# Kernel optimization log

Measured on AMD Instinct MI355X. Metric: run time of the kernel, lower is better.

## Reference

```python
import jax, jax.numpy as jnp
import numpy as np

# edge types from metadata: (src_type, 'to', dst_type)
NODE_SRC = [0, 1, 2, 3, 0, 1, 2, 1, 3, 1]
NODE_DST = [0, 1, 2, 3, 1, 0, 1, 2, 1, 3]
N_NODES = 30000
N_EDGES = 400000
HEADS1 = 8


def _han_conv(xs, edges, proj_W, proj_b, att_src, att_dst, k_W, k_b, q, heads):
    """Faithful port of torch_geometric HANConv (eval mode, dropout off)."""
    out_ch = proj_W.shape[-1]
    D = out_ch // heads
    N = xs[0].shape[0]
    # per-node-type projection -> [N, H, D]
    h = [(xs[t] @ proj_W[t] + proj_b[t]).reshape(N, heads, D) for t in range(4)]
    outs = {t: [] for t in range(4)}
    for e in range(10):
        s, d = NODE_SRC[e], NODE_DST[e]
        row, col = edges[e, 0], edges[e, 1]
        a_src = (h[s] * att_src[e]).sum(-1)  # [N, H]
        a_dst = (h[d] * att_dst[e]).sum(-1)  # [N, H]
        alpha = jax.nn.leaky_relu(a_src[row] + a_dst[col], 0.2)  # [E, H]
        # segment softmax over incoming edges of each dst node
        amax = jax.ops.segment_max(alpha, col, num_segments=N)
        ex = jnp.exp(alpha - amax[col])
        denom = jax.ops.segment_sum(ex, col, num_segments=N)
        w = ex / (denom[col] + 1e-16)
        msg = h[s][row] * w[:, :, None]  # [E, H, D]
        agg = jax.ops.segment_sum(msg, col, num_segments=N).reshape(N, out_ch)
        outs[d].append(jax.nn.relu(agg))
    # semantic-level attention fusion across relations ending at each node type
    res = []
    for t in range(4):
        stk = jnp.stack(outs[t])  # [M, N, C]
        score = (q * jnp.tanh(stk @ k_W + k_b).mean(axis=1)).sum(-1)  # [M]
        sattn = jax.nn.softmax(score)
        res.append((sattn[:, None, None] * stk).sum(0))  # [N, C]
    return res


def setup_inputs() -> dict:
    key = jax.random.key(0)
    ks = jax.random.split(key, 24)
    inp = {}
    for t in range(4):
        inp[f"x{t}"] = jax.random.normal(ks[t], (N_NODES, 256), dtype=jnp.float32)
    inp["edges"] = jax.random.randint(ks[4], (10, 2, N_EDGES), 0, N_NODES, dtype=jnp.int32)
    s = 0.05
    inp["proj1_W"] = jax.random.normal(ks[5], (4, 256, 128), dtype=jnp.float32) * s
    inp["proj1_b"] = jax.random.normal(ks[6], (4, 128), dtype=jnp.float32) * s
    inp["att1_src"] = jax.random.normal(ks[7], (10, 8, 16), dtype=jnp.float32) * s
    inp["att1_dst"] = jax.random.normal(ks[8], (10, 8, 16), dtype=jnp.float32) * s
    inp["k1_W"] = jax.random.normal(ks[9], (128, 128), dtype=jnp.float32) * s
    inp["k1_b"] = jax.random.normal(ks[10], (128,), dtype=jnp.float32) * s
    inp["q1"] = jax.random.normal(ks[11], (128,), dtype=jnp.float32) * s
    inp["proj2_W"] = jax.random.normal(ks[12], (4, 128, 32), dtype=jnp.float32) * s
    inp["proj2_b"] = jax.random.normal(ks[13], (4, 32), dtype=jnp.float32) * s
    inp["att2_src"] = jax.random.normal(ks[14], (10, 1, 32), dtype=jnp.float32) * s
    inp["att2_dst"] = jax.random.normal(ks[15], (10, 1, 32), dtype=jnp.float32) * s
    inp["k2_W"] = jax.random.normal(ks[16], (32, 32), dtype=jnp.float32) * s
    inp["k2_b"] = jax.random.normal(ks[17], (32,), dtype=jnp.float32) * s
    inp["q2"] = jax.random.normal(ks[18], (32,), dtype=jnp.float32) * s
    return inp


def reference(x0, x1, x2, x3, edges,
              proj1_W, proj1_b, att1_src, att1_dst, k1_W, k1_b, q1,
              proj2_W, proj2_b, att2_src, att2_dst, k2_W, k2_b, q2):
    # eval mode: all F.dropout calls are identity
    xs = [x0, x1, x2, x3]
    h = _han_conv(xs, edges, proj1_W, proj1_b, att1_src, att1_dst, k1_W, k1_b, q1, HEADS1)
    h = [jax.nn.elu(v) for v in h]
    o = _han_conv(h, edges, proj2_W, proj2_b, att2_src, att2_dst, k2_W, k2_b, q2, 1)
    # final per-node softmax over channel dim for each node type; stack since all N equal
    return jnp.stack([jax.nn.softmax(v, axis=1) for v in o])  # [4, N, 32]
```

## Files before the change

### kernel.cpp

```cpp
#include <hip/hip_runtime.h>
#include <hip/hip_fp16.h>

#define NN 30000
#define NE 400000
#define NBUCK 59
#define BPR 98
#define EPB 4096
#define CAPREG 12288
#define BCAP 12288

__constant__ int d_SRC[10] = {0,1,2,3,0,1,2,1,3,1};
__constant__ int d_DST[10] = {0,1,2,3,1,0,1,2,1,3};
__constant__ int d_RORD[10] = {1,5,7,9,0,4,2,6,3,8};
__constant__ int d_GORD[10] = {0,4,1,5,7,9,2,6,3,8};
__constant__ int d_FCNT[4] = {2,4,2,2};
__constant__ int d_FREL[4][4] = {{0,5,0,0},{1,4,6,8},{2,7,0,0},{3,9,0,0}};

typedef _Float16 f16x8 __attribute__((ext_vector_type(8)));
typedef float f32x4 __attribute__((ext_vector_type(4)));

template<int BN, bool AF16>
__global__ __launch_bounds__(256)
void mgemm_k(const float* __restrict__ A, long sA,
             const float* __restrict__ B, long sB,
             const float* __restrict__ bias, long sBias,
             float* __restrict__ C, long sC,
             int M, int K, int N, int relu_a, int epi)
{
    constexpr int BM = 64, BK = 32;
    constexpr int NF = BN / 16;
    constexpr int LDK = BK + 8;
    const int z = blockIdx.z;
    const _Float16* __restrict__ Ah = (const _Float16*)A;
    if constexpr (AF16) Ah += (long)z * sA; else A += (long)z * sA;
    B += (long)z * sB;
    bias += (long)z * sBias;
    C += (long)z * sC;
    const int m0 = blockIdx.x * BM;
    const int n0 = blockIdx.y * BN;
    const int tid = threadIdx.x;
    const int wv = tid >> 6;
    const int l  = tid & 63;
    const int fm = l & 15;
    const int fg = l >> 4;

    __shared__ _Float16 As[BM][LDK];
    __shared__ _Float16 Bs[BN][LDK];
    __shared__ float red[4][BN];

    f32x4 acc[NF];
#pragma unroll
    for (int f = 0; f < NF; ++f) acc[f] = (f32x4){0.f, 0.f, 0.f, 0.f};

    const int arow = tid >> 2;
    const int akc  = (tid & 3) << 3;
    const int grow = m0 + arow;

    for (int k0 = 0; k0 < K; k0 += BK) {
        f16x8 ap;
        if (grow < M) {
            if constexpr (AF16) {
                ap = *(const f16x8*)(Ah + (long)grow * K + k0 + akc);
                if (relu_a) {
#pragma unroll
                    for (int j = 0; j < 8; ++j)
                        ap[j] = ap[j] > (_Float16)0.f ? ap[j] : (_Float16)0.f;
                }
            } else {
                const float* aq = A + (long)grow * K + k0 + akc;
                float4 u0 = *(const float4*)aq;
                float4 u1 = *(const float4*)(aq + 4);
                float v[8] = {u0.x, u0.y, u0.z, u0.w, u1.x, u1.y, u1.z, u1.w};
                if (relu_a) {
#pragma unroll
                    for (int j = 0; j < 8; ++j) v[j] = fmaxf(v[j], 0.f);
                }
#pragma unroll
                for (int j = 0; j < 8; ++j) ap[j] = (_Float16)v[j];
            }
        } else {
#pragma unroll
            for (int j = 0; j < 8; ++j) ap[j] = (_Float16)0.f;
        }
        *(f16x8*)&As[arow][akc] = ap;

        if constexpr (BN == 64) {
            const int bk = tid >> 4;
            const int bn = (tid & 15) << 2;
#pragma unroll
            for (int kk = 0; kk < 2; ++kk) {
                int kr = bk + kk * 16;
                float4 u = *(const float4*)(B + (long)(k0 + kr) * N + n0 + bn);
                Bs[bn + 0][kr] = (_Float16)u.x;
                Bs[bn + 1][kr] = (_Float16)u.y;
                Bs[bn + 2][kr] = (_Float16)u.z;
                Bs[bn + 3][kr] = (_Float16)u.w;
            }
        } else {
            const int bk = tid >> 3;
            const int bn = (tid & 7) << 2;
            float4 u = *(const float4*)(B + (long)(k0 + bk) * N + n0 + bn);
            Bs[bn + 0][bk] = (_Float16)u.x;
            Bs[bn + 1][bk] = (_Float16)u.y;
            Bs[bn + 2][bk] = (_Float16)u.z;
            Bs[bn + 3][bk] = (_Float16)u.w;
        }
        __syncthreads();

        f16x8 a = *(const f16x8*)&As[wv * 16 + fm][fg * 8];
#pragma unroll
        for (int f = 0; f < NF; ++f) {
            f16x8 b = *(const f16x8*)&Bs[f * 16 + fm][fg * 8];
            acc[f] = __builtin_amdgcn_mfma_f32_16x16x32_f16(a, b, acc[f], 0, 0, 0);
        }
        __syncthreads();
    }

    if (epi == 0) {
#pragma unroll
        for (int f = 0; f < NF; ++f) {
            float bz = bias[n0 + f * 16 + fm];
#pragma unroll
            for (int i = 0; i < 4; ++i) {
                int gr = m0 + wv * 16 + fg * 4 + i;
                if (gr < M) C[(long)gr * N + n0 + f * 16 + fm] = acc[f][i] + bz;
            }
        }
    } else if (epi == 2) {
        __half* Ch = (__half*)C;
#pragma unroll
        for (int f = 0; f < NF; ++f) {
            float bz = bias[n0 + f * 16 + fm];
#pragma unroll
            for (int i = 0; i < 4; ++i) {
                int gr = m0 + wv * 16 + fg * 4 + i;
                if (gr < M) Ch[(long)gr * N + n0 + f * 16 + fm] = __float2half(acc[f][i] + bz);
            }
        }
    } else {
#pragma unroll
        for (int f = 0; f < NF; ++f) {
            float bz = bias[n0 + f * 16 + fm];
            float s = 0.f;
#pragma unroll
            for (int i = 0; i < 4; ++i) {
                int gr = m0 + wv * 16 + fg * 4 + i;
                if (gr < M) s += tanhf(acc[f][i] + bz);
            }
            s += __shfl_xor(s, 16, 64);
            s += __shfl_xor(s, 32, 64);
            if (fg == 0) red[wv][f * 16 + fm] = s;
        }
        __syncthreads();
        if (tid < BN) {
            float s = red[0][tid] + red[1][tid] + red[2][tid] + red[3][tid];
            unsafeAtomicAdd(&C[n0 + tid], s);
        }
    }
}

__global__ __launch_bounds__(256)
void init_bincur(int* __restrict__ binCur)
{
    int i = blockIdx.x * 256 + threadIdx.x;
    if (i < 10 * NBUCK) binCur[i] = (i % NBUCK) * CAPREG;
}

__global__ __launch_bounds__(256)
void csr_binA(const int* __restrict__ edges, int* __restrict__ binCur,
              unsigned* __restrict__ binned)
{
    __shared__ int lcnt[NBUCK];
    __shared__ int gbase[NBUCK];
    int rel = blockIdx.x / BPR;
    int blk = blockIdx.x - rel * BPR;
    int base = blk * EPB;
    int tid = threadIdx.x;
    for (int b = tid; b < NBUCK; b += 256) lcnt[b] = 0;
    __syncthreads();
    const int* er = edges + (long)rel * 2 * NE;
    const int* ec = er + NE;
    unsigned pk[16];
    unsigned mt[16];
#pragma unroll
    for (int k = 0; k < 16; ++k) {
        int i = base + k * 256 + tid;
        if (i < NE) {
            int r = er[i];
            int c = ec[i];
            int b = c >> 9;
            int lo = atomicAdd(&lcnt[b], 1);
            pk[k] = ((unsigned)c << 15) | (unsigned)r;
            mt[k] = ((unsigned)b << 16) | (unsigned)lo;
        } else {
            mt[k] = 0xFFFFFFFFu;
        }
    }
    __syncthreads();
    if (tid < NBUCK) gbase[tid] = atomicAdd(&binCur[rel * NBUCK + tid], lcnt[tid]);
    __syncthreads();
    unsigned* bn = binned + (long)rel * NBUCK * CAPREG;
#pragma unroll
    for (int k = 0; k < 16; ++k) {
        if (mt[k] != 0xFFFFFFFFu) {
            int b = mt[k] >> 16;
            int lo = mt[k] & 0xFFFF;
            bn[gbase[b] + lo] = pk[k];
        }
    }
}

__global__ __launch_bounds__(64)
void bucket_scan(const int* __restrict__ binCur, int* __restrict__ bbase,
                 int* __restrict__ off_all)
{
    int rel = blockIdx.x;
    int t = threadIdx.x;
    __shared__ int c[64];
    int v = (t < NBUCK) ? (binCur[rel * NBUCK + t] - t * CAPREG) : 0;
    c[t] = v;
    __syncthreads();
    for (int d = 1; d < 64; d <<= 1) {
        int u = (t >= d) ? c[t - d] : 0;
        __syncthreads();
        c[t] += u;
        __syncthreads();
    }
    if (t < NBUCK) bbase[rel * NBUCK + t] = c[t] - v;
    if (t == 0) off_all[rel * (NN + 1) + NN] = NE;
}

__global__ __launch_bounds__(256)
void csr_binB(const int* __restrict__ binCur, const int* __restrict__ bbase,
              const unsigned* __restrict__ binned,
              int* __restrict__ off_all, int* __restrict__ rows)
{
    __shared__ int cntS[512];
    __shared__ int lcur[512];
    __shared__ int part[256];
    __shared__ int buf[BCAP];
    int rel = blockIdx.x / NBUCK;
    int bkt = blockIdx.x - rel * NBUCK;
    const unsigned* bn = binned + ((long)rel * NBUCK + bkt) * CAPREG;
    int* off = off_all + rel * (NN + 1);
    int* rw = rows + (long)rel * NE;
    int cnt = binCur[rel * NBUCK + bkt] - bkt * CAPREG;
    int gbase = bbase[rel * NBUCK + bkt];
    int nb0 = bkt << 9;
    int nb1 = min(nb0 + 512, NN);
    int nloc = nb1 - nb0;
    int tid = threadIdx.x;

    cntS[tid] = 0; cntS[tid + 256] = 0;
    __syncthreads();
    for (int j = tid; j < cnt; j += 256) {
        int c = (int)(bn[j] >> 15);
        atomicAdd(&cntS[c - nb0], 1);
    }
    __syncthreads();
    int c0 = cntS[2 * tid], c1 = cntS[2 * tid + 1];
    part[tid] = c0 + c1;
    __syncthreads();
    for (int d = 1; d < 256; d <<= 1) {
        int u = (tid >= d) ? part[tid - d] : 0;
        __syncthreads();
        part[tid] += u;
        __syncthreads();
    }
    int pre = (tid == 0) ? 0 : part[tid - 1];
    cntS[2 * tid] = pre;
    cntS[2 * tid + 1] = pre + c0;
    __syncthreads();
    for (int i = tid; i < nloc; i += 256) off[nb0 + i] = gbase + cntS[i];
    lcur[tid] = cntS[tid]; lcur[tid + 256] = cntS[tid + 256];
    __syncthreads();
    if (cnt <= BCAP) {
        for (int j = tid; j < cnt; j += 256) {
            unsigned p = bn[j];
            int r = (int)(p & 0x7FFF);
            int c = (int)(p >> 15);
            int pos = atomicAdd(&lcur[c - nb0], 1);
            buf[pos] = r;
        }
        __syncthreads();
        for (int i = tid; i < cnt; i += 256) rw[gbase + i] = buf[i];
    } else {
        for (int j = tid; j < cnt; j += 256) {
            unsigned p = bn[j];
            int r = (int)(p & 0x7FFF);
            int c = (int)(p >> 15);
            int pos = atomicAdd(&lcur[c - nb0], 1);
            rw[gbase + pos] = r;
        }
    }
}

__global__ __launch_bounds__(256)
void attn_dots1(const __half* __restrict__ h1h,
                const float* __restrict__ att_src,
                const float* __restrict__ att_dst,
                float* __restrict__ asrc, float* __restrict__ adst)
{
    int gid = blockIdx.x * 256 + threadIdx.x;
    int wave = gid >> 6;
    int lane = gid & 63;
    if (wave >= 4 * NN) return;
    int t = wave / NN;
    int n = wave - t * NN;
    __half2 hh = *(const __half2*)&h1h[(long)(t * NN + n) * 128 + 2 * lane];
    float2 hv = __half22float2(hh);
    const int SRCc[10] = {0,1,2,3,0,1,2,1,3,1};
    const int DSTc[10] = {0,1,2,3,1,0,1,2,1,3};
#pragma unroll
    for (int e = 0; e < 10; ++e) {
        if (SRCc[e] == t) {
            float2 av = *(const float2*)&att_src[e * 128 + 2 * lane];
            float p = hv.x * av.x + hv.y * av.y;
#pragma unroll
            for (int off = 1; off < 8; off <<= 1) p += __shfl_xor(p, off, 64);
            if ((lane & 7) == 0) asrc[(long)(e * NN + n) * 8 + (lane >> 3)] = p;
        }
        if (DSTc[e] == t) {
            float2 bv = *(const float2*)&att_dst[e * 128 + 2 * lane];
            float p = hv.x * bv.x + hv.y * bv.y;
#pragma unroll
            for (int off = 1; off < 8; off <<= 1) p += __shfl_xor(p, off, 64);
            if ((lane & 7) == 0) adst[(long)(e * NN + n) * 8 + (lane >> 3)] = p;
        }
    }
}

__global__ __launch_bounds__(256)
void gather_agg1_all(const int* __restrict__ csr_off, const int* __restrict__ csr_rows,
                     const float* __restrict__ asrc1, const float* __restrict__ adst1,
                     const __half* __restrict__ h1h, __half* __restrict__ slots16)
{
    int e = d_GORD[blockIdx.y];
    int node = blockIdx.x * 4 + (threadIdx.x >> 6);
    int lane = threadIdx.x & 63;
    if (node >= NN) return;
    const int* off = csr_off + e * (NN + 1);
    const int* rows = csr_rows + (long)e * NE;
    const float* asrc_e = asrc1 + (long)e * NN * 8;
    const float* adst_e = adst1 + (long)e * NN * 8;
    const __half* h1s = h1h + (long)d_SRC[e] * NN * 128;
    __half* out = slots16 + (long)e * NN * 128;

    const int hB = lane >> 3;
    const int hA = lane & 7;
    const int eA = lane >> 3;
    int beg = off[node], end = off[node + 1];
    float adA = adst_e[node * 8 + hA];
    float den = 1e-16f;
    float accx = 0.f, accy = 0.f;
    for (int j0 = beg; j0 < end; j0 += 8) {
        int jj = j0 + eA;
        bool ok = jj < end;
        int r = rows[ok ? jj : beg];
        float a = asrc_e[r * 8 + hA] + adA;
        a = a > 0.f ? a : 0.2f * a;
        float w = ok ? __expf(a) : 0.f;
        int cnt = end - j0;
        if (cnt >= 8) {
#pragma unroll
            for (int i = 0; i < 8; ++i) {
                float wi = __shfl(w, i * 8 + hB, 64);
                int ri = __shfl(r, i * 8, 64);
                float2 v = __half22float2(*(const __half2*)&h1s[(long)ri * 128 + 2 * lane]);
                den += wi;
                accx += wi * v.x;
                accy += wi * v.y;
            }
        } else {
            for (int i = 0; i < cnt; ++i) {
                float wi = __shfl(w, i * 8 + hB, 64);
                int ri = __shfl(r, i * 8, 64);
                float2 v = __half22float2(*(const __half2*)&h1s[(long)ri * 128 + 2 * lane]);
                den += wi;
                accx += wi * v.x;
                accy += wi * v.y;
            }
        }
    }
    float inv = 1.0f / den;
    *(__half2*)&out[(long)node * 128 + 2 * lane] = __floats2half2_rn(accx * inv, accy * inv);
}

__global__ __launch_bounds__(256)
void fusion_all(const __half* __restrict__ slots16, const float* __restrict__ sattn,
                __half* __restrict__ h1f)
{
    int t = blockIdx.y;
    int idx = blockIdx.x * 256 + threadIdx.x;
    if (idx >= NN * 32) return;
    int c4 = idx & 31;
    int n = idx >> 5;
    long off = (long)n * 128 + c4 * 4;
    int cnt = d_FCNT[t];
    float o0 = 0.f, o1 = 0.f, o2 = 0.f, o3 = 0.f;
    for (int j = 0; j < cnt; ++j) {
        int e = d_FREL[t][j];
        float w = sattn[e];
        const __half* p = slots16 + (long)e * NN * 128 + off;
        float2 v01 = __half22float2(*(const __half2*)p);
        float2 v23 = __half22float2(*(const __half2*)(p + 2));
        o0 += w * fmaxf(v01.x, 0.f);
        o1 += w * fmaxf(v01.y, 0.f);
        o2 += w * fmaxf(v23.x, 0.f);
        o3 += w * fmaxf(v23.y, 0.f);
    }
    o0 = o0 > 0.f ? o0 : __expf(o0) - 1.f;
    o1 = o1 > 0.f ? o1 : __expf(o1) - 1.f;
    o2 = o2 > 0.f ? o2 : __expf(o2) - 1.f;
    o3 = o3 > 0.f ? o3 : __expf(o3) - 1.f;
    __half* q = h1f + (long)t * NN * 128 + off;
    *(__half2*)q = __floats2half2_rn(o0, o1);
    *(__half2*)(q + 2) = __floats2half2_rn(o2, o3);
}

__global__ __launch_bounds__(256)
void attn_dots2(const __half* __restrict__ h2h,
                const float* __restrict__ att_src,
                const float* __restrict__ att_dst,
                float* __restrict__ asrc, float* __restrict__ adst)
{
    int gid = blockIdx.x * 256 + threadIdx.x;
    int p = gid >> 5;
    int l = gid & 31;
    if (p >= 10 * NN) return;
    int e = p / NN, n = p - e * NN;
    int s = d_SRC[e], d = d_DST[e];
    float hs = __half2float(h2h[(long)(s * NN + n) * 32 + l]);
    float hd = __half2float(h2h[(long)(d * NN + n) * 32 + l]);
    float ps = hs * att_src[e * 32 + l];
    float pd = hd * att_dst[e * 32 + l];
#pragma unroll
    for (int off = 1; off < 32; off <<= 1) {
        ps += __shfl_xor(ps, off, 64);
        pd += __shfl_xor(pd, off, 64);
    }
    if (l == 0) { asrc[e * NN + n] = ps; adst[e * NN + n] = pd; }
}

__global__ __launch_bounds__(256)
void gather_agg2(const int* __restrict__ csr_off, const int* __restrict__ csr_rows,
                 const __half* __restrict__ h2h,
                 const float* __restrict__ asrc, const float* __restrict__ adst,
                 float* __restrict__ agg2)
{
    int e = d_RORD[blockIdx.y];
    int node = blockIdx.x * 8 + (threadIdx.x >> 5);
    int lane = threadIdx.x & 31;
    if (node >= NN) return;
    const int* off = csr_off + e * (NN + 1);
    const int* rows = csr_rows + (long)e * NE;
    const __half* h2s = h2h + (long)d_SRC[e] * NN * 32;
    const float* as = asrc + e * NN;
    float ad = adst[e * NN + node];
    int beg = off[node], end = off[node + 1];
    float den = 1e-16f;
    float acc = 0.f;
    for (int j0 = beg; j0 < end; j0 += 32) {
        int jj = j0 + lane;
        bool ok = jj < end;
        int r = rows[ok ? jj : beg];
        float a = as[r] + ad;
        a = a > 0.f ? a : 0.2f * a;
        float w = ok ? __expf(a) : 0.f;
        int cnt = min(32, end - j0);
        int i = 0;
        for (; i + 3 < cnt; i += 4) {
            float w0 = __shfl(w, i, 32);
            float w1 = __shfl(w, i + 1, 32);
            float w2 = __shfl(w, i + 2, 32);
            float w3 = __shfl(w, i + 3, 32);
            int r0 = __shfl(r, i, 32);
            int r1 = __shfl(r, i + 1, 32);
            int r2 = __shfl(r, i + 2, 32);
            int r3 = __shfl(r, i + 3, 32);
            float v0 = __half2float(h2s[(long)r0 * 32 + lane]);
            float v1 = __half2float(h2s[(long)r1 * 32 + lane]);
            float v2 = __half2float(h2s[(long)r2 * 32 + lane]);
            float v3 = __half2float(h2s[(long)r3 * 32 + lane]);
            den += (w0 + w1) + (w2 + w3);
            acc += w0 * v0 + w1 * v1 + w2 * v2 + w3 * v3;
        }
        for (; i < cnt; ++i) {
            float wi = __shfl(w, i, 32);
            int ri = __shfl(r, i, 32);
            den += wi;
            acc += wi * __half2float(h2s[(long)ri * 32 + lane]);
        }
    }
    agg2[((long)e * NN + node) * 32 + lane] = acc / den;
}

__global__ void score_all_k(const float* __restrict__ colsum, const float* __restrict__ q,
                            float* __restrict__ sattn, int C)
{
    __shared__ float sc[10];
    int tid = threadIdx.x;
    if (tid < 10) {
        float s = 0.f;
        for (int c = 0; c < C; ++c) s += q[c] * colsum[tid * C + c];
        sc[tid] = s / (float)NN;
    }
    __syncthreads();
    if (tid < 4) {
        float mx = -1e30f;
        for (int m = 0; m < 10; ++m) if (d_DST[m] == tid) mx = fmaxf(mx, sc[m]);
        float ex[10];
        float sum = 0.f;
        for (int m = 0; m < 10; ++m) {
            ex[m] = 0.f;
            if (d_DST[m] == tid) { ex[m] = __expf(sc[m] - mx); sum += ex[m]; }
        }
        for (int m = 0; m < 10; ++m) if (d_DST[m] == tid) sattn[m] = ex[m] / sum;
    }
}

__global__ __launch_bounds__(256)
void final_softmax(const float* __restrict__ agg, const float* __restrict__ sattn,
                   float* __restrict__ out)
{
    int gid = blockIdx.x * 256 + threadIdx.x;
    int c = gid & 31;
    int p = gid >> 5;
    if (p >= 4 * NN) return;
    int t = p / NN, n = p - t * NN;
    float f = 0.f;
    for (int m = 0; m < 10; ++m) {
        if (d_DST[m] != t) continue;
        f += sattn[m] * fmaxf(agg[(long)(m * NN + n) * 32 + c], 0.f);
    }
    float mx = f;
#pragma unroll
    for (int off = 1; off < 32; off <<= 1) mx = fmaxf(mx, __shfl_xor(mx, off, 64));
    float ex = __expf(f - mx);
    float sm = ex;
#pragma unroll
    for (int off = 1; off < 32; off <<= 1) sm += __shfl_xor(sm, off, 64);
    out[(long)(t * NN + n) * 32 + c] = ex / sm;
}

extern "C" void kernel_launch(void* const* d_in, const int* in_sizes, int n_in,
                              void* d_out, int out_size, void* d_ws, size_t ws_size,
                              hipStream_t stream) {
    const float* x[4] = {
        (const float*)d_in[0], (const float*)d_in[1],
        (const float*)d_in[2], (const float*)d_in[3]};
    const int* edges = (const int*)d_in[4];
    const float* W1    = (const float*)d_in[5];
    const float* b1    = (const float*)d_in[6];
    const float* att1s = (const float*)d_in[7];
    const float* att1d = (const float*)d_in[8];
    const float* k1W   = (const float*)d_in[9];
    const float* k1b   = (const float*)d_in[10];
    const float* q1    = (const float*)d_in[11];
    const float* W2    = (const float*)d_in[12];
    const float* b2    = (const float*)d_in[13];
    const float* att2s = (const float*)d_in[14];
    const float* att2d = (const float*)d_in[15];
    const float* k2W   = (const float*)d_in[16];
    const float* k2b   = (const float*)d_in[17];
    const float* q2    = (const float*)d_in[18];

    float* W = (float*)d_ws;
    __half* h1h    = (__half*)W;
    __half* h1f    = (__half*)W;
    __half* h2h    = (__half*)(W + 7680000);
    __half* slots16 = (__half*)(W + 15360000);
    float* agg2    = W + 15360000;
    unsigned* binned = (unsigned*)(W + 15360000);
    int*   binCur  = (int*)(W + 15360000 + 7249920);
    int*   bbase   = binCur + 640;
    float* asrc1   = W + 34560000;
    float* adst1   = W + 36960000;
    float* asrc2   = W + 36960000;
    float* adst2   = W + 37260000;
    float* colsum1 = W + 39360000;
    float* sattn1  = W + 39361280;
    float* colsum2 = W + 39361296;
    float* sattn2  = W + 39361616;
    int*   csr_off = (int*)(W + 39361640);
    int*   csr_row = csr_off + 300016;

    init_bincur<<<3, 256, 0, stream>>>(binCur);
    csr_binA<<<BPR * 10, 256, 0, stream>>>(edges, binCur, binned);
    bucket_scan<<<10, 64, 0, stream>>>(binCur, bbase, csr_off);
    csr_binB<<<NBUCK * 10, 256, 0, stream>>>(binCur, bbase, binned, csr_off, csr_row);

    hipMemsetAsync(colsum1, 0, 1632L * 4, stream);

    for (int t = 0; t < 4; ++t) {
        mgemm_k<64, false><<<dim3(469, 2, 1), 256, 0, stream>>>(
            x[t], 0, W1 + (long)t * 256 * 128, 0, b1 + t * 128, 0,
            (float*)(h1h + (long)t * NN * 128), 0, NN, 256, 128, 0, 2);
    }

    attn_dots1<<<30000, 256, 0, stream>>>(h1h, att1s, att1d, asrc1, adst1);

    gather_agg1_all<<<dim3(7500, 10), 256, 0, stream>>>(
        csr_off, csr_row, asrc1, adst1, h1h, slots16);

    mgemm_k<64, true><<<dim3(469, 2, 10), 256, 0, stream>>>(
        (const float*)slots16, (long)NN * 128, k1W, 0, k1b, 0,
        colsum1, 128, NN, 128, 128, 1, 1);
    score_all_k<<<1, 64, 0, stream>>>(colsum1, q1, sattn1, 128);

    fusion_all<<<dim3(3750, 4), 256, 0, stream>>>(slots16, sattn1, h1f);

    mgemm_k<32, true><<<dim3(469, 1, 4), 256, 0, stream>>>(
        (const float*)h1f, (long)NN * 128, W2, 128L * 32, b2, 32,
        (float*)h2h, (long)NN * 16, NN, 128, 32, 0, 2);

    attn_dots2<<<37500, 256, 0, stream>>>(h2h, att2s, att2d, asrc2, adst2);
    gather_agg2<<<dim3(3750, 10), 256, 0, stream>>>(
        csr_off, csr_row, h2h, asrc2, adst2, agg2);

    mgemm_k<32, false><<<dim3(469, 1, 10), 256, 0, stream>>>(
        agg2, 960000L, k2W, 0, k2b, 0, colsum2, 32L, NN, 32, 32, 1, 1);
    score_all_k<<<1, 64, 0, stream>>>(colsum2, q2, sattn2, 32);
    final_softmax<<<15000, 256, 0, stream>>>(agg2, sattn2, (float*)d_out);
}
```

Measured before the change: 801.8 us.

## Widen gather loads to 8 bytes and store layer-2 aggregates in fp16

In layer 1, the gather kernel now splits each 64-lane wave into two half-waves that take alternate edges, each lane loading four fp16 values, and combines the halves with a cross-lane shuffle. The layer-2 gather moves from one 32-lane group per node to one 64-lane wave per node, with eight edge slots of eight lanes each, 8-byte loads and a shuffle reduction. The layer-2 aggregate buffer changes from fp32 to fp16, so the following GEMM and the final softmax read half the bytes. The aim is fewer, wider memory transactions and less traffic, at the cost of extra shuffle reductions, idle lanes on low-degree nodes, and fp16 rounding of the layer-2 aggregates.

```diff
diff --git a/kernel.cpp b/kernel.cpp
--- a/kernel.cpp
+++ b/kernel.cpp
@@ -18,6 +18,8 @@
 
 typedef _Float16 f16x8 __attribute__((ext_vector_type(8)));
 typedef float f32x4 __attribute__((ext_vector_type(4)));
+
+struct __attribute__((aligned(8))) h2x2 { __half2 a, b; };
 
 template<int BN, bool AF16>
 __global__ __launch_bounds__(256)
@@ -346,13 +348,28 @@
     const __half* h1s = h1h + (long)d_SRC[e] * NN * 128;
     __half* out = slots16 + (long)e * NN * 128;
 
-    const int hB = lane >> 3;
-    const int hA = lane & 7;
-    const int eA = lane >> 3;
+    const int g   = lane >> 5;
+    const int sub = lane & 31;
+    const int hv  = sub >> 2;
+    const int eA  = lane >> 3;
+    const int hA  = lane & 7;
     int beg = off[node], end = off[node + 1];
     float adA = adst_e[node * 8 + hA];
-    float den = 1e-16f;
-    float accx = 0.f, accy = 0.f;
+    float den = (g == 0) ? 1e-16f : 0.f;
+    float a0 = 0.f, a1 = 0.f, a2 = 0.f, a3 = 0.f;
+
+#define GA1_PAIR(i)                                                              \
+    {                                                                            \
+        int e0 = 2 * (i) + g;                                                    \
+        float wi = __shfl(w, e0 * 8 + hv, 64);                                   \
+        int ri = __shfl(r, e0 * 8, 64);                                          \
+        h2x2 v = *(const h2x2*)(h1s + (long)ri * 128 + 4 * sub);                 \
+        float2 f0 = __half22float2(v.a);                                         \
+        float2 f1 = __half22float2(v.b);                                         \
+        den += wi;                                                               \
+        a0 += wi * f0.x; a1 += wi * f0.y; a2 += wi * f1.x; a3 += wi * f1.y;      \
+    }
+
     for (int j0 = beg; j0 < end; j0 += 8) {
         int jj = j0 + eA;
         bool ok = jj < end;
@@ -362,28 +379,25 @@
         float w = ok ? __expf(a) : 0.f;
         int cnt = end - j0;
         if (cnt >= 8) {
-#pragma unroll
-            for (int i = 0; i < 8; ++i) {
-                float wi = __shfl(w, i * 8 + hB, 64);
-                int ri = __shfl(r, i * 8, 64);
-                float2 v = __half22float2(*(const __half2*)&h1s[(long)ri * 128 + 2 * lane]);
-                den += wi;
-                accx += wi * v.x;
-                accy += wi * v.y;
-            }
+            GA1_PAIR(0) GA1_PAIR(1) GA1_PAIR(2) GA1_PAIR(3)
         } else {
-            for (int i = 0; i < cnt; ++i) {
-                float wi = __shfl(w, i * 8 + hB, 64);
-                int ri = __shfl(r, i * 8, 64);
-                float2 v = __half22float2(*(const __half2*)&h1s[(long)ri * 128 + 2 * lane]);
-                den += wi;
-                accx += wi * v.x;
-                accy += wi * v.y;
-            }
-        }
-    }
-    float inv = 1.0f / den;
-    *(__half2*)&out[(long)node * 128 + 2 * lane] = __floats2half2_rn(accx * inv, accy * inv);
+            int pr = (cnt + 1) >> 1;
+            for (int i = 0; i < pr; ++i) GA1_PAIR(i)
+        }
+    }
+#undef GA1_PAIR
+    a0 += __shfl_xor(a0, 32, 64);
+    a1 += __shfl_xor(a1, 32, 64);
+    a2 += __shfl_xor(a2, 32, 64);
+    a3 += __shfl_xor(a3, 32, 64);
+    den += __shfl_xor(den, 32, 64);
+    if (g == 0) {
+        float inv = 1.0f / den;
+        h2x2 o;
+        o.a = __floats2half2_rn(a0 * inv, a1 * inv);
+        o.b = __floats2half2_rn(a2 * inv, a3 * inv);
+        *(h2x2*)(out + (long)node * 128 + 4 * sub) = o;
+    }
 }
 
 __global__ __launch_bounds__(256)
@@ -446,53 +460,67 @@
 void gather_agg2(const int* __restrict__ csr_off, const int* __restrict__ csr_rows,
                  const __half* __restrict__ h2h,
                  const float* __restrict__ asrc, const float* __restrict__ adst,
-                 float* __restrict__ agg2)
+                 __half* __restrict__ agg2h)
 {
     int e = d_RORD[blockIdx.y];
-    int node = blockIdx.x * 8 + (threadIdx.x >> 5);
-    int lane = threadIdx.x & 31;
+    int node = blockIdx.x * 4 + (threadIdx.x >> 6);
+    int lane = threadIdx.x & 63;
     if (node >= NN) return;
     const int* off = csr_off + e * (NN + 1);
     const int* rows = csr_rows + (long)e * NE;
     const __half* h2s = h2h + (long)d_SRC[e] * NN * 32;
     const float* as = asrc + e * NN;
+    const int slot = lane >> 3;
+    const int sub = lane & 7;
     float ad = adst[e * NN + node];
     int beg = off[node], end = off[node + 1];
-    float den = 1e-16f;
-    float acc = 0.f;
-    for (int j0 = beg; j0 < end; j0 += 32) {
+    float den = (lane < 8) ? 1e-16f : 0.f;
+    float a0 = 0.f, a1 = 0.f, a2 = 0.f, a3 = 0.f;
+
+#define GA2_STEP(i)                                                              \
+    {                                                                            \
+        int e0 = (i) * 8 + slot;                                                 \
+        float wi = __shfl(w, e0, 64);                                            \
+        int ri = __shfl(r, e0, 64);                                              \
+        h2x2 v = *(const h2x2*)(h2s + (long)ri * 32 + 4 * sub);                  \
+        float2 f0 = __half22float2(v.a);                                         \
+        float2 f1 = __half22float2(v.b);                                         \
+        den += wi;                                                               \
+        a0 += wi * f0.x; a1 += wi * f0.y; a2 += wi * f1.x; a3 += wi * f1.y;      \
+    }
+
+    for (int j0 = beg; j0 < end; j0 += 64) {
         int jj = j0 + lane;
         bool ok = jj < end;
         int r = rows[ok ? jj : beg];
         float a = as[r] + ad;
         a = a > 0.f ? a : 0.2f * a;
         float w = ok ? __expf(a) : 0.f;
-        int cnt = min(32, end - j0);
-        int i = 0;
-        for (; i + 3 < cnt; i += 4) {
-            float w0 = __shfl(w, i, 32);
-            float w1 = __shfl(w, i + 1, 32);
-            float w2 = __shfl(w, i + 2, 32);
-            float w3 = __shfl(w, i + 3, 32);
-            int r0 = __shfl(r, i, 32);
-            int r1 = __shfl(r, i + 1, 32);
-            int r2 = __shfl(r, i + 2, 32);
-            int r3 = __shfl(r, i + 3, 32);
-            float v0 = __half2float(h2s[(long)r0 * 32 + lane]);
-            float v1 = __half2float(h2s[(long)r1 * 32 + lane]);
-            float v2 = __half2float(h2s[(long)r2 * 32 + lane]);
-            float v3 = __half2float(h2s[(long)r3 * 32 + lane]);
-            den += (w0 + w1) + (w2 + w3);
-            acc += w0 * v0 + w1 * v1 + w2 * v2 + w3 * v3;
-        }
-        for (; i < cnt; ++i) {
-            float wi = __shfl(w, i, 32);
-            int ri = __shfl(r, i, 32);
-            den += wi;
-            acc += wi * __half2float(h2s[(long)ri * 32 + lane]);
-        }
-    }
-    agg2[((long)e * NN + node) * 32 + lane] = acc / den;
+        int cnt = end - j0;
+        if (cnt >= 64) {
+            GA2_STEP(0) GA2_STEP(1) GA2_STEP(2) GA2_STEP(3)
+            GA2_STEP(4) GA2_STEP(5) GA2_STEP(6) GA2_STEP(7)
+        } else {
+            int it = (cnt + 7) >> 3;
+            for (int i = 0; i < it; ++i) GA2_STEP(i)
+        }
+    }
+#undef GA2_STEP
+#pragma unroll
+    for (int m = 8; m < 64; m <<= 1) {
+        a0 += __shfl_xor(a0, m, 64);
+        a1 += __shfl_xor(a1, m, 64);
+        a2 += __shfl_xor(a2, m, 64);
+        a3 += __shfl_xor(a3, m, 64);
+        den += __shfl_xor(den, m, 64);
+    }
+    if (lane < 8) {
+        float inv = 1.0f / den;
+        h2x2 o;
+        o.a = __floats2half2_rn(a0 * inv, a1 * inv);
+        o.b = __floats2half2_rn(a2 * inv, a3 * inv);
+        *(h2x2*)(agg2h + ((long)e * NN + node) * 32 + 4 * sub) = o;
+    }
 }
 
 __global__ void score_all_k(const float* __restrict__ colsum, const float* __restrict__ q,
@@ -520,7 +548,7 @@
 }
 
 __global__ __launch_bounds__(256)
-void final_softmax(const float* __restrict__ agg, const float* __restrict__ sattn,
+void final_softmax(const __half* __restrict__ agg, const float* __restrict__ sattn,
                    float* __restrict__ out)
 {
     int gid = blockIdx.x * 256 + threadIdx.x;
@@ -531,7 +559,7 @@
     float f = 0.f;
     for (int m = 0; m < 10; ++m) {
         if (d_DST[m] != t) continue;
-        f += sattn[m] * fmaxf(agg[(long)(m * NN + n) * 32 + c], 0.f);
+        f += sattn[m] * fmaxf(__half2float(agg[(long)(m * NN + n) * 32 + c]), 0.f);
     }
     float mx = f;
 #pragma unroll
@@ -570,7 +598,7 @@
     __half* h1f    = (__half*)W;
     __half* h2h    = (__half*)(W + 7680000);
     __half* slots16 = (__half*)(W + 15360000);
-    float* agg2    = W + 15360000;
+    __half* agg2h  = (__half*)(W + 15360000);
     unsigned* binned = (unsigned*)(W + 15360000);
     int*   binCur  = (int*)(W + 15360000 + 7249920);
     int*   bbase   = binCur + 640;
@@ -615,11 +643,12 @@
         (float*)h2h, (long)NN * 16, NN, 128, 32, 0, 2);
 
     attn_dots2<<<37500, 256, 0, stream>>>(h2h, att2s, att2d, asrc2, adst2);
-    gather_agg2<<<dim3(3750, 10), 256, 0, stream>>>(
-        csr_off, csr_row, h2h, asrc2, adst2, agg2);
-
-    mgemm_k<32, false><<<dim3(469, 1, 10), 256, 0, stream>>>(
-        agg2, 960000L, k2W, 0, k2b, 0, colsum2, 32L, NN, 32, 32, 1, 1);
+    gather_agg2<<<dim3(7500, 10), 256, 0, stream>>>(
+        csr_off, csr_row, h2h, asrc2, adst2, agg2h);
+
+    mgemm_k<32, true><<<dim3(469, 1, 10), 256, 0, stream>>>(
+        (const float*)agg2h, (long)NN * 32, k2W, 0, k2b, 0,
+        colsum2, 32L, NN, 32, 32, 1, 1);
     score_all_k<<<1, 64, 0, stream>>>(colsum2, q2, sattn2, 32);
-    final_softmax<<<15000, 256, 0, stream>>>(agg2, sattn2, (float*)d_out);
-}
+    final_softmax<<<15000, 256, 0, stream>>>(agg2h, sattn2, (float*)d_out);
+}
```

New measurement: 820.6 us. 1.02x slower.
